# Kernel optimization log

Hardware: AMD Instinct MI355X
Metric: run time of the kernel (lower is better)

Reference implementation:

```python
import jax, jax.numpy as jnp
import numpy as np

TOTAL_POINTS = 1048576
C = 256
B = 512


def setup_inputs() -> dict:
    key = jax.random.key(0)
    k1, k2 = jax.random.split(key)
    values = jax.random.normal(k1, (TOTAL_POINTS, C), dtype=jnp.float32)
    # sorted segment ids == flattened ragged list membership (List[(N_i,C)])
    segment_ids = jnp.sort(jax.random.randint(k2, (TOTAL_POINTS,), 0, B, dtype=jnp.int32))
    return {"values": values, "segment_ids": segment_ids, "num_segments": B}


def reference(values, segment_ids, num_segments):
    # torch.stack([x.sum(dim=0) for x in inputs]) == segmented sum over the
    # flattened point axis -> (B, C). Single fused pass, indices are sorted.
    return jax.ops.segment_sum(values, segment_ids,
                               num_segments=num_segments,
                               indices_are_sorted=True)
```

## Files before the change

kernel.cpp:

```cpp
#include <hip/hip_runtime.h>


#define TOTAL_POINTS 1048576
#define NCOLS 256
#define NSEGS 512
#define SPLIT 4
#define NBLOCKS (NSEGS * SPLIT)

typedef float v4 __attribute__((ext_vector_type(4)));

__global__ __launch_bounds__(256) void segsum_kernel(
    const v4* __restrict__ vals,
    const int* __restrict__ segids,
    float* __restrict__ out)
{
    const int c4 = threadIdx.x & 63;
    const int rg = threadIdx.x >> 6;
    const int seg = blockIdx.x >> 2;
    const int q   = blockIdx.x & 3;

    int lo0 = 0, hi0 = TOTAL_POINTS;
    int lo1 = 0, hi1 = TOTAL_POINTS;
    #pragma unroll
    for (int it = 0; it < 20; ++it) {
        const int m0 = (lo0 + hi0) >> 1;
        const int m1 = (lo1 + hi1) >> 1;
        const int a = segids[m0];
        const int b = segids[m1];
        if (a < seg)     lo0 = m0 + 1; else hi0 = m0;
        if (b < seg + 1) lo1 = m1 + 1; else hi1 = m1;
    }
    const int rows   = lo1 - lo0;
    const int rstart = lo0 + ((rows * q) >> 2);
    const int rend   = lo0 + ((rows * (q + 1)) >> 2);

    const int n = rend - (rstart + rg);
    const int iters = (n > 0) ? ((n + 3) >> 2) : 0;

    v4 acc = (v4)(0.f);
    const v4* p = vals + (long)(rstart + rg) * 64 + c4;
    #pragma unroll 8
    for (int i = 0; i < iters; ++i) {
        acc += p[0];
        p += 4 * 64;
    }

    if (iters > 0) {
        float* o = out + (long)seg * NCOLS + (c4 << 2);
        atomicAdd(o + 0, acc.x);
        atomicAdd(o + 1, acc.y);
        atomicAdd(o + 2, acc.z);
        atomicAdd(o + 3, acc.w);
    }
}

extern "C" void kernel_launch(void* const* d_in, const int* in_sizes, int n_in,
                              void* d_out, int out_size, void* d_ws, size_t ws_size,
                              hipStream_t stream) {
    const float* vals = (const float*)d_in[0];
    const int* segids = (const int*)d_in[1];
    float* out = (float*)d_out;

    hipMemsetAsync(out, 0, (size_t)out_size * sizeof(float), stream);

    segsum_kernel<<<NBLOCKS, 256, 0, stream>>>(
        (const v4*)vals, segids, out);
}
```

Measured before the change: 1.330 ms.

## Use one 1024-thread block per segment with shared-memory reduction, drop atomics and memset

Each segment is now handled by a single 16-wave block instead of four 4-wave blocks. Per-wave partial sums are combined in shared memory and written directly, so the float atomics and the separate memset launch are no longer needed. The grid is smaller (512 blocks of 1024 threads), which may lower occupancy balance across CUs, and the binary search now runs redundantly in more threads per segment.

```diff
diff --git a/kernel.cpp b/kernel.cpp
--- a/kernel.cpp
+++ b/kernel.cpp
@@ -4,20 +4,19 @@
 #define TOTAL_POINTS 1048576
 #define NCOLS 256
 #define NSEGS 512
-#define SPLIT 4
-#define NBLOCKS (NSEGS * SPLIT)
+#define NWAVES 16
+#define BLOCK (NWAVES * 64)
 
 typedef float v4 __attribute__((ext_vector_type(4)));
 
-__global__ __launch_bounds__(256) void segsum_kernel(
+__global__ __launch_bounds__(BLOCK) void segsum_kernel(
     const v4* __restrict__ vals,
     const int* __restrict__ segids,
     float* __restrict__ out)
 {
     const int c4 = threadIdx.x & 63;
-    const int rg = threadIdx.x >> 6;
-    const int seg = blockIdx.x >> 2;
-    const int q   = blockIdx.x & 3;
+    const int w  = threadIdx.x >> 6;
+    const int seg = blockIdx.x;
 
     int lo0 = 0, hi0 = TOTAL_POINTS;
     int lo1 = 0, hi1 = TOTAL_POINTS;
@@ -30,27 +29,27 @@
         if (a < seg)     lo0 = m0 + 1; else hi0 = m0;
         if (b < seg + 1) lo1 = m1 + 1; else hi1 = m1;
     }
-    const int rows   = lo1 - lo0;
-    const int rstart = lo0 + ((rows * q) >> 2);
-    const int rend   = lo0 + ((rows * (q + 1)) >> 2);
+    const int rows = lo1 - lo0;
 
-    const int n = rend - (rstart + rg);
-    const int iters = (n > 0) ? ((n + 3) >> 2) : 0;
+    const int n = rows - w;
+    const int iters = (n > 0) ? ((n + NWAVES - 1) >> 4) : 0;
 
     v4 acc = (v4)(0.f);
-    const v4* p = vals + (long)(rstart + rg) * 64 + c4;
+    const v4* p = vals + (long)(lo0 + w) * 64 + c4;
     #pragma unroll 8
     for (int i = 0; i < iters; ++i) {
         acc += p[0];
-        p += 4 * 64;
+        p += NWAVES * 64;
     }
 
-    if (iters > 0) {
-        float* o = out + (long)seg * NCOLS + (c4 << 2);
-        atomicAdd(o + 0, acc.x);
-        atomicAdd(o + 1, acc.y);
-        atomicAdd(o + 2, acc.z);
-        atomicAdd(o + 3, acc.w);
+    __shared__ v4 red[NWAVES][64];
+    red[w][c4] = acc;
+    __syncthreads();
+    if (w == 0) {
+        #pragma unroll
+        for (int j = 1; j < NWAVES; ++j)
+            acc += red[j][c4];
+        *((v4*)(out + (long)seg * NCOLS) + c4) = acc;
     }
 }
 
@@ -61,8 +60,6 @@
     const int* segids = (const int*)d_in[1];
     float* out = (float*)d_out;
 
-    hipMemsetAsync(out, 0, (size_t)out_size * sizeof(float), stream);
-
-    segsum_kernel<<<NBLOCKS, 256, 0, stream>>>(
+    segsum_kernel<<<NSEGS, BLOCK, 0, stream>>>(
         (const v4*)vals, segids, out);
 }
```

Measured after the change: 1.315 ms. No clear change (-1.1%).
